# Kernel tuning notes

Hardware: AMD Instinct MI355X
Metric: run time of the kernel (lower is better)

Reference implementation:

```python
import jax, jax.numpy as jnp
import numpy as np

N, H, V = 8192, 1024, 32000
IGNORE_INDEX = -100
LABEL_SMOOTHING = 0.0
LOGIT_SCALE = 1.0


def setup_inputs() -> dict:
    key = jax.random.key(0)
    k1, k2, k3 = jax.random.split(key, 3)
    x = jax.random.normal(k1, (N, H), dtype=jnp.float32)
    weight = jax.random.normal(k2, (V, H), dtype=jnp.float32) * 0.02
    bias = jnp.zeros((V,), dtype=jnp.float32)
    target = jax.random.randint(k3, (N,), 0, V, dtype=jnp.int64)
    return {"x": x, "weight": weight, "bias": bias, "target": target}


def reference(x, weight, bias, target):
    # logits: [N, V]; fused kernel never materializes this fully, but math is identical
    logits = (x @ weight.T + bias) * LOGIT_SCALE
    lse = jax.nn.logsumexp(logits.astype(jnp.float32), axis=-1)  # [N]
    valid = target != IGNORE_INDEX
    safe_t = jnp.where(valid, target, 0)
    tgt_logit = jnp.take_along_axis(logits, safe_t[:, None], axis=-1)[:, 0]
    loss_i = lse - tgt_logit
    if LABEL_SMOOTHING > 0:
        eps = LABEL_SMOOTHING / V
        z = (-eps * logits).sum(-1)
        loss_i = loss_i * (1.0 - LABEL_SMOOTHING) + (z + LABEL_SMOOTHING * lse)
    loss_i = jnp.where(valid, loss_i, 0.0)
    total = jnp.maximum(valid.sum(), 1)
    # reduction == 'mean': each per-token loss divided by total, then summed
    return loss_i.sum() / total
```

## Files before the change

kernel.cpp:

```cpp
#include <hip/hip_runtime.h>
#include <math.h>

typedef int    intx8    __attribute__((ext_vector_type(8)));
typedef float  floatx16 __attribute__((ext_vector_type(16)));

#define N_ROWS 8192
#define H_DIM  1024
#define V_DIM  32000
#define V_PAD  32768
#define IGNORE_INDEX (-100)

#define S_SPLITS 16
#define TILES_PER_SPLIT 16
#define BM 256
#define BN 128
#define BK 128

#define LOG2E 1.4426950408889634f
#define LN2   0.6931471805599453f

__global__ __launch_bounds__(256) void convert_fp8(const float* __restrict__ in,
                                                   unsigned char* __restrict__ out,
                                                   int Rstride, float scale) {
  const int r = blockIdx.x * 256 + threadIdx.x;
  const int u = blockIdx.y;
  const float4* src = (const float4*)(in + (size_t)r * H_DIM + u * 16);
  uint4 res;
#pragma unroll
  for (int j = 0; j < 4; ++j) {
    const float4 v = src[j];
    int p = __builtin_amdgcn_cvt_pk_fp8_f32(v.x * scale, v.y * scale, 0, false);
    p = __builtin_amdgcn_cvt_pk_fp8_f32(v.z * scale, v.w * scale, p, true);
    ((int*)&res)[j] = p;
  }
  *(uint4*)(out + ((size_t)u * Rstride + r) * 16) = res;
}

__global__ __launch_bounds__(256) void pad_bias(const float* __restrict__ bias,
                                                float* __restrict__ biasp) {
  const int i = blockIdx.x * 256 + threadIdx.x;
  biasp[i] = (i < V_DIM) ? bias[i] * LOG2E : -1e30f;
}

__global__ __launch_bounds__(256, 2) void flce_main(const unsigned char* __restrict__ xs,
                                                    const unsigned char* __restrict__ wsb,
                                                    const float* __restrict__ biasp,
                                                    float* __restrict__ partials) {
  __shared__ __align__(16) unsigned char smA[8 * 256 * 16];
  __shared__ __align__(16) unsigned char smB[8 * 128 * 16];

  const int tid  = threadIdx.x;
  const int lane = tid & 63;
  const int w    = tid >> 6;
  const int l31  = lane & 31;
  const int half = lane >> 5;
  const int wr   = w * 64;
  const int row0 = blockIdx.x * BM;
  const int sidx = blockIdx.y;

  float l_state[32];
#pragma unroll
  for (int i = 0; i < 32; ++i) l_state[i] = 0.f;

#pragma unroll 1
  for (int ct = 0; ct < TILES_PER_SPLIT; ++ct) {
    const int n0 = (sidx * TILES_PER_SPLIT + ct) * BN;
    floatx16 acc[2][4];
#pragma unroll
    for (int mb = 0; mb < 2; ++mb)
#pragma unroll
      for (int nb = 0; nb < 4; ++nb)
#pragma unroll
        for (int i = 0; i < 16; ++i) acc[mb][nb][i] = 0.f;

#pragma unroll 1
    for (int k0i = 0; k0i < H_DIM / BK; ++k0i) {
      const int ub = k0i * 8;
      __syncthreads();
#pragma unroll
      for (int j = 0; j < 8; ++j) {
        const int c = j * 4 + w;
        const int u = c >> 2;
        const int rb = c & 3;
        __builtin_amdgcn_global_load_lds(
            (const __attribute__((address_space(1))) void*)(xs + ((size_t)(ub + u) * N_ROWS + row0 + rb * 64 + lane) * 16),
            (__attribute__((address_space(3))) void*)(smA + ((u * 256 + rb * 64 + lane) * 16)),
            16, 0, 0);
      }
#pragma unroll
      for (int j = 0; j < 4; ++j) {
        const int c = j * 4 + w;
        const int u = c >> 1;
        const int rb = c & 1;
        __builtin_amdgcn_global_load_lds(
            (const __attribute__((address_space(1))) void*)(wsb + ((size_t)(ub + u) * V_PAD + n0 + rb * 64 + lane) * 16),
            (__attribute__((address_space(3))) void*)(smB + ((u * 128 + rb * 64 + lane) * 16)),
            16, 0, 0);
      }
      __syncthreads();

#pragma unroll
      for (int s2 = 0; s2 < 2; ++s2) {
        const int ua = s2 * 4 + half * 2;
        union { intx8 v; uint4 q[2]; } a[2], b[4];
#pragma unroll
        for (int mb = 0; mb < 2; ++mb) {
          a[mb].q[0] = *(const uint4*)(smA + ((ua * 256 + wr + mb * 32 + l31) * 16));
          a[mb].q[1] = *(const uint4*)(smA + (((ua + 1) * 256 + wr + mb * 32 + l31) * 16));
        }
#pragma unroll
        for (int nb = 0; nb < 4; ++nb) {
          b[nb].q[0] = *(const uint4*)(smB + ((ua * 128 + nb * 32 + l31) * 16));
          b[nb].q[1] = *(const uint4*)(smB + (((ua + 1) * 128 + nb * 32 + l31) * 16));
        }
#pragma unroll
        for (int mb = 0; mb < 2; ++mb)
#pragma unroll
          for (int nb = 0; nb < 4; ++nb)
            acc[mb][nb] = __builtin_amdgcn_mfma_scale_f32_32x32x64_f8f6f4(
                a[mb].v, b[nb].v, acc[mb][nb],
                0, 0,
                0, 0x7F7F7F7F,
                0, 0x7F7F7F7F);
      }
    }

    float bnb[4];
#pragma unroll
    for (int nb = 0; nb < 4; ++nb) bnb[nb] = biasp[n0 + nb * 32 + l31];
#pragma unroll
    for (int mb = 0; mb < 2; ++mb)
#pragma unroll
      for (int r = 0; r < 16; ++r) {
        float s = exp2f(acc[mb][0][r] + bnb[0]) + exp2f(acc[mb][1][r] + bnb[1])
                + exp2f(acc[mb][2][r] + bnb[2]) + exp2f(acc[mb][3][r] + bnb[3]);
        l_state[mb * 16 + r] += s;
      }
  }

#pragma unroll
  for (int s = 0; s < 32; ++s) {
    float v = l_state[s];
#pragma unroll
    for (int off = 1; off < 32; off <<= 1) v += __shfl_xor(v, off, 64);
    l_state[s] = v;
  }

  if (l31 == 0) {
#pragma unroll
    for (int s = 0; s < 32; ++s) {
      const int mb = s >> 4, r = s & 15;
      const int row = wr + mb * 32 + 4 * half + (r & 3) + 8 * (r >> 2);
      partials[(size_t)(row0 + row) * S_SPLITS + sidx] = l_state[s];
    }
  }
}

__global__ __launch_bounds__(256) void tgt_kernel(const float* __restrict__ x,
                                                  const float* __restrict__ wgt,
                                                  const float* __restrict__ bias,
                                                  const int* __restrict__ target,
                                                  float* __restrict__ tgt_logit) {
  const int r = blockIdx.x * 4 + (threadIdx.x >> 6);
  const int lane = threadIdx.x & 63;
  const int t = target[r];
  const int tt = (t == IGNORE_INDEX) ? 0 : t;
  const float4* xr = (const float4*)(x + (size_t)r * H_DIM);
  const float4* wr = (const float4*)(wgt + (size_t)tt * H_DIM);
  float acc = 0.f;
#pragma unroll
  for (int i = 0; i < 4; ++i) {
    const float4 a = xr[lane + i * 64];
    const float4 b = wr[lane + i * 64];
    acc += a.x * b.x + a.y * b.y + a.z * b.z + a.w * b.w;
  }
#pragma unroll
  for (int off = 32; off >= 1; off >>= 1) acc += __shfl_xor(acc, off, 64);
  if (lane == 0) tgt_logit[r] = acc + bias[tt];
}

__global__ __launch_bounds__(256) void loss_rows(const float* __restrict__ partials,
                                                 const float* __restrict__ tgt_logit,
                                                 const int* __restrict__ target,
                                                 float* __restrict__ bsums) {
  const int r = blockIdx.x * 256 + threadIdx.x;
  float l = 0.f;
#pragma unroll
  for (int s = 0; s < S_SPLITS; ++s) l += partials[(size_t)r * S_SPLITS + s];
  const float lse = LN2 * __log2f(l);
  const bool valid = (target[r] != IGNORE_INDEX);
  float loss = valid ? (lse - tgt_logit[r]) : 0.f;
  float cnt  = valid ? 1.f : 0.f;
  const int lane = threadIdx.x & 63;
  const int w = threadIdx.x >> 6;
#pragma unroll
  for (int off = 32; off >= 1; off >>= 1) {
    loss += __shfl_xor(loss, off, 64);
    cnt  += __shfl_xor(cnt, off, 64);
  }
  __shared__ float sl[4], sc[4];
  if (lane == 0) { sl[w] = loss; sc[w] = cnt; }
  __syncthreads();
  if (threadIdx.x == 0) {
    float S = 0.f, C = 0.f;
    for (int i = 0; i < 4; ++i) { S += sl[i]; C += sc[i]; }
    bsums[blockIdx.x] = S;
    bsums[32 + blockIdx.x] = C;
  }
}

__global__ void finalize(const float* __restrict__ bsums, float* __restrict__ out) {
  const int t = threadIdx.x;
  float s = (t < 32) ? bsums[t] : 0.f;
  float c = (t < 32) ? bsums[32 + t] : 0.f;
#pragma unroll
  for (int off = 32; off >= 1; off >>= 1) {
    s += __shfl_xor(s, off, 64);
    c += __shfl_xor(c, off, 64);
  }
  if (t == 0) out[0] = s / fmaxf(c, 1.f);
}

extern "C" void kernel_launch(void* const* d_in, const int* in_sizes, int n_in,
                              void* d_out, int out_size, void* d_ws, size_t ws_size,
                              hipStream_t stream) {
  const float* x    = (const float*)d_in[0];
  const float* wgt  = (const float*)d_in[1];
  const float* bias = (const float*)d_in[2];
  const int*   tgt  = (const int*)d_in[3];
  float* out = (float*)d_out;

  char* ws = (char*)d_ws;
  const size_t XS8 = (size_t)N_ROWS * H_DIM;
  const size_t WS8 = (size_t)V_PAD * H_DIM;
  const size_t BP  = (size_t)V_PAD * 4;
  const size_t PB  = (size_t)N_ROWS * S_SPLITS * 4;
  unsigned char* xs8 = (unsigned char*)ws;
  unsigned char* ws8 = (unsigned char*)(ws + XS8);
  float* biasp    = (float*)(ws + XS8 + WS8);
  float* partials = (float*)(ws + XS8 + WS8 + BP);
  float* tgt_lg   = (float*)(ws + XS8 + WS8 + BP + PB);
  float* bsums    = (float*)(ws + XS8 + WS8 + BP + PB + (size_t)N_ROWS * 4);

  convert_fp8<<<dim3(N_ROWS / 256, H_DIM / 16), 256, 0, stream>>>(x, xs8, N_ROWS, LOG2E);
  convert_fp8<<<dim3(V_DIM / 256, H_DIM / 16), 256, 0, stream>>>(wgt, ws8, V_PAD, 1.0f);
  pad_bias<<<V_PAD / 256, 256, 0, stream>>>(bias, biasp);
  tgt_kernel<<<N_ROWS / 4, 256, 0, stream>>>(x, wgt, bias, tgt, tgt_lg);
  flce_main<<<dim3(N_ROWS / BM, S_SPLITS), 256, 0, stream>>>(xs8, ws8, biasp, partials);
  loss_rows<<<N_ROWS / 256, 256, 0, stream>>>(partials, tgt_lg, tgt, bsums);
  finalize<<<1, 64, 0, stream>>>(bsums, out);
}
```

Baseline: 504.2 us.

## Double-buffer LDS tiles with prefetch two steps ahead across column tiles

Replaces the synchronous load-then-compute K loop with a two-buffer software pipeline using BK=64 steps. Global-to-LDS loads for step+2 are issued right after the current fragments are read into registers, and the pipeline runs continuously across column tiles so loads overlap the MFMAs. It also stages the bias slice into LDS once at kernel start, uses manual vmcnt/lgkmcnt waits with raw barriers, and raises wave priority around the MFMA block. Costs are more barriers per K, a larger LDS footprint that may affect occupancy, and fragile hand-counted wait values.

```diff
diff --git a/kernel.cpp b/kernel.cpp
--- a/kernel.cpp
+++ b/kernel.cpp
@@ -14,7 +14,9 @@
 #define TILES_PER_SPLIT 16
 #define BM 256
 #define BN 128
-#define BK 128
+#define BK 64
+#define KSTEPS 16
+#define TOTAL_STEPS (TILES_PER_SPLIT * KSTEPS)
 
 #define LOG2E 1.4426950408889634f
 #define LN2   0.6931471805599453f
@@ -42,12 +44,86 @@
   biasp[i] = (i < V_DIM) ? bias[i] * LOG2E : -1e30f;
 }
 
+
+#define STAGE(ST, CUR) do {                                                              \
+    const int _ss = (ST);                                                                \
+    const int _ks = _ss & 15;                                                            \
+    const int _ct = _ss >> 4;                                                            \
+    const int _ub = _ks * 4;                                                             \
+    const int _n0 = (sidx * TILES_PER_SPLIT + _ct) * BN;                                 \
+    _Pragma("unroll")                                                                    \
+    for (int _j = 0; _j < 4; ++_j) {                                                     \
+      const int _c = _j * 4 + w, _u = _c >> 2, _rb = _c & 3;                             \
+      __builtin_amdgcn_global_load_lds(                                                  \
+          (const __attribute__((address_space(1))) void*)(xs +                           \
+              ((size_t)(_ub + _u) * N_ROWS + row0 + _rb * 64 + lane) * 16),              \
+          (__attribute__((address_space(3))) void*)(smA + (CUR) * (4 * 256 * 16) +       \
+              (_u * 256 + _rb * 64 + lane) * 16),                                        \
+          16, 0, 0);                                                                     \
+    }                                                                                    \
+    _Pragma("unroll")                                                                    \
+    for (int _j = 0; _j < 2; ++_j) {                                                     \
+      const int _c = _j * 4 + w, _u = _c >> 1, _rb = _c & 1;                             \
+      __builtin_amdgcn_global_load_lds(                                                  \
+          (const __attribute__((address_space(1))) void*)(wsb +                          \
+              ((size_t)(_ub + _u) * V_PAD + _n0 + _rb * 64 + lane) * 16),                \
+          (__attribute__((address_space(3))) void*)(smB + (CUR) * (4 * 128 * 16) +       \
+              (_u * 128 + _rb * 64 + lane) * 16),                                        \
+          16, 0, 0);                                                                     \
+    }                                                                                    \
+  } while (0)
+
+#define DO_STEP(ST, CUR) do {                                                            \
+    const int _st = (ST);                                                                \
+                     \
+    if (_st < TOTAL_STEPS - 1) asm volatile("s_waitcnt vmcnt(6)" ::: "memory");          \
+    else                       asm volatile("s_waitcnt vmcnt(0)" ::: "memory");          \
+    __builtin_amdgcn_sched_barrier(0);                                                   \
+    __builtin_amdgcn_s_barrier();                     \
+    union { intx8 v; uint4 q[2]; } a[2], b[4];                                           \
+    {                                                                                    \
+      const int ua = half * 2;                                                           \
+      _Pragma("unroll")                                                                  \
+      for (int mb = 0; mb < 2; ++mb) {                                                   \
+        a[mb].q[0] = *(const uint4*)(smA + (CUR) * (4 * 256 * 16) +                      \
+                                     ((ua * 256 + wr + mb * 32 + l31) * 16));            \
+        a[mb].q[1] = *(const uint4*)(smA + (CUR) * (4 * 256 * 16) +                      \
+                                     (((ua + 1) * 256 + wr + mb * 32 + l31) * 16));      \
+      }                                                                                  \
+      _Pragma("unroll")                                                                  \
+      for (int nb = 0; nb < 4; ++nb) {                                                   \
+        b[nb].q[0] = *(const uint4*)(smB + (CUR) * (4 * 128 * 16) +                      \
+                                     ((ua * 128 + nb * 32 + l31) * 16));                 \
+        b[nb].q[1] = *(const uint4*)(smB + (CUR) * (4 * 128 * 16) +                      \
+                                     (((ua + 1) * 128 + nb * 32 + l31) * 16));           \
+      }                                                                                  \
+    }                                                                                    \
+    asm volatile("s_waitcnt lgkmcnt(0)" ::: "memory");        \
+    __builtin_amdgcn_sched_barrier(0);                                                   \
+    __builtin_amdgcn_s_barrier();                   \
+    __builtin_amdgcn_sched_barrier(0);                                                   \
+    if (_st + 2 < TOTAL_STEPS) STAGE(_st + 2, CUR);           \
+    __builtin_amdgcn_sched_barrier(0);                                                   \
+    __builtin_amdgcn_s_setprio(1);                                                       \
+    _Pragma("unroll")                                                                    \
+    for (int mb = 0; mb < 2; ++mb)                                                       \
+      _Pragma("unroll")                                                                  \
+      for (int nb = 0; nb < 4; ++nb)                                                     \
+        acc[mb][nb] = __builtin_amdgcn_mfma_scale_f32_32x32x64_f8f6f4(                   \
+            a[mb].v, b[nb].v, acc[mb][nb],                                               \
+            0, 0,                                                  \
+            0, 0x7F7F7F7F,                                            \
+            0, 0x7F7F7F7F);                                           \
+    __builtin_amdgcn_s_setprio(0);                                                       \
+  } while (0)
+
 __global__ __launch_bounds__(256, 2) void flce_main(const unsigned char* __restrict__ xs,
                                                     const unsigned char* __restrict__ wsb,
                                                     const float* __restrict__ biasp,
                                                     float* __restrict__ partials) {
-  __shared__ __align__(16) unsigned char smA[8 * 256 * 16];
-  __shared__ __align__(16) unsigned char smB[8 * 128 * 16];
+  __shared__ __align__(16) unsigned char smA[2 * 4 * 256 * 16];
+  __shared__ __align__(16) unsigned char smB[2 * 4 * 128 * 16];
+  __shared__ __align__(16) float sbias[TILES_PER_SPLIT * BN];
 
   const int tid  = threadIdx.x;
   const int lane = tid & 63;
@@ -62,9 +138,20 @@
 #pragma unroll
   for (int i = 0; i < 32; ++i) l_state[i] = 0.f;
 
+#pragma unroll
+  for (int j = 0; j < 2; ++j) {
+    const int c = j * 4 + w;
+    __builtin_amdgcn_global_load_lds(
+        (const __attribute__((address_space(1))) void*)(biasp +
+            (size_t)sidx * (TILES_PER_SPLIT * BN) + c * 256 + lane * 4),
+        (__attribute__((address_space(3))) void*)(sbias + c * 256 + lane * 4),
+        16, 0, 0);
+  }
+  STAGE(0, 0);
+  STAGE(1, 1);
+
 #pragma unroll 1
   for (int ct = 0; ct < TILES_PER_SPLIT; ++ct) {
-    const int n0 = (sidx * TILES_PER_SPLIT + ct) * BN;
     floatx16 acc[2][4];
 #pragma unroll
     for (int mb = 0; mb < 2; ++mb)
@@ -74,60 +161,15 @@
         for (int i = 0; i < 16; ++i) acc[mb][nb][i] = 0.f;
 
 #pragma unroll 1
-    for (int k0i = 0; k0i < H_DIM / BK; ++k0i) {
-      const int ub = k0i * 8;
-      __syncthreads();
-#pragma unroll
-      for (int j = 0; j < 8; ++j) {
-        const int c = j * 4 + w;
-        const int u = c >> 2;
-        const int rb = c & 3;
-        __builtin_amdgcn_global_load_lds(
-            (const __attribute__((address_space(1))) void*)(xs + ((size_t)(ub + u) * N_ROWS + row0 + rb * 64 + lane) * 16),
-            (__attribute__((address_space(3))) void*)(smA + ((u * 256 + rb * 64 + lane) * 16)),
-            16, 0, 0);
-      }
-#pragma unroll
-      for (int j = 0; j < 4; ++j) {
-        const int c = j * 4 + w;
-        const int u = c >> 1;
-        const int rb = c & 1;
-        __builtin_amdgcn_global_load_lds(
-            (const __attribute__((address_space(1))) void*)(wsb + ((size_t)(ub + u) * V_PAD + n0 + rb * 64 + lane) * 16),
-            (__attribute__((address_space(3))) void*)(smB + ((u * 128 + rb * 64 + lane) * 16)),
-            16, 0, 0);
-      }
-      __syncthreads();
-
-#pragma unroll
-      for (int s2 = 0; s2 < 2; ++s2) {
-        const int ua = s2 * 4 + half * 2;
-        union { intx8 v; uint4 q[2]; } a[2], b[4];
-#pragma unroll
-        for (int mb = 0; mb < 2; ++mb) {
-          a[mb].q[0] = *(const uint4*)(smA + ((ua * 256 + wr + mb * 32 + l31) * 16));
-          a[mb].q[1] = *(const uint4*)(smA + (((ua + 1) * 256 + wr + mb * 32 + l31) * 16));
-        }
-#pragma unroll
-        for (int nb = 0; nb < 4; ++nb) {
-          b[nb].q[0] = *(const uint4*)(smB + ((ua * 128 + nb * 32 + l31) * 16));
-          b[nb].q[1] = *(const uint4*)(smB + (((ua + 1) * 128 + nb * 32 + l31) * 16));
-        }
-#pragma unroll
-        for (int mb = 0; mb < 2; ++mb)
-#pragma unroll
-          for (int nb = 0; nb < 4; ++nb)
-            acc[mb][nb] = __builtin_amdgcn_mfma_scale_f32_32x32x64_f8f6f4(
-                a[mb].v, b[nb].v, acc[mb][nb],
-                0, 0,
-                0, 0x7F7F7F7F,
-                0, 0x7F7F7F7F);
-      }
+    for (int ks2 = 0; ks2 < 8; ++ks2) {
+      const int st0 = ct * 16 + ks2 * 2;
+      DO_STEP(st0, 0);
+      DO_STEP(st0 + 1, 1);
     }
 
     float bnb[4];
 #pragma unroll
-    for (int nb = 0; nb < 4; ++nb) bnb[nb] = biasp[n0 + nb * 32 + l31];
+    for (int nb = 0; nb < 4; ++nb) bnb[nb] = sbias[ct * BN + nb * 32 + l31];
 #pragma unroll
     for (int mb = 0; mb < 2; ++mb)
 #pragma unroll
```

Measured after the change: 548.1 us. +8.7%, slower.

## Triple-buffer LDS loads with one barrier per K-step and prefetch across tiles

Applied to the files above, without the earlier changes.

Replaces the two-barrier, single-buffer K loop with a three-stage LDS ring that uses BK=64 and a single barrier per step. Global-to-LDS loads are issued two steps ahead, including across column-tile boundaries, and synchronisation relies on explicit vmcnt waits. Bias values are preloaded into LDS once per block, and MFMA issue is given raised wave priority. The aim is to hide global load latency behind MFMA work and drop the barrier stalls. In exchange, each step does less compute per barrier and the vmcnt accounting is fragile.

```diff
diff --git a/kernel.cpp b/kernel.cpp
--- a/kernel.cpp
+++ b/kernel.cpp
@@ -14,7 +14,12 @@
 #define TILES_PER_SPLIT 16
 #define BM 256
 #define BN 128
-#define BK 128
+#define BK 64
+#define KSTEPS 16
+#define TOTAL_STEPS (TILES_PER_SPLIT * KSTEPS)
+
+#define ABUF_SZ (4 * 256 * 16)
+#define BBUF_SZ (4 * 128 * 16)
 
 #define LOG2E 1.4426950408889634f
 #define LN2   0.6931471805599453f
@@ -42,12 +47,42 @@
   biasp[i] = (i < V_DIM) ? bias[i] * LOG2E : -1e30f;
 }
 
+
+#define STAGE(ST, BUF) do {                                                              \
+    const int _ss = (ST);                                                                \
+    const int _ks = _ss & 15;                                                            \
+    const int _ct = _ss >> 4;                                                            \
+    const int _ub = _ks * 4;                                                             \
+    const int _n0 = (sidx * TILES_PER_SPLIT + _ct) * BN;                                 \
+    unsigned char* _dA = smA + (BUF) * ABUF_SZ;                                          \
+    unsigned char* _dB = smB + (BUF) * BBUF_SZ;                                          \
+    _Pragma("unroll")                                                                    \
+    for (int _j = 0; _j < 4; ++_j) {                                                     \
+      const int _c = _j * 4 + w, _u = _c >> 2, _rb = _c & 3;                             \
+      __builtin_amdgcn_global_load_lds(                                                  \
+          (const __attribute__((address_space(1))) void*)(xs +                           \
+              ((size_t)(_ub + _u) * N_ROWS + row0 + _rb * 64 + lane) * 16),              \
+          (__attribute__((address_space(3))) void*)(_dA + (_u * 256 + _rb * 64 + lane) * 16), \
+          16, 0, 0);                                                                     \
+    }                                                                                    \
+    _Pragma("unroll")                                                                    \
+    for (int _j = 0; _j < 2; ++_j) {                                                     \
+      const int _c = _j * 4 + w, _u = _c >> 1, _rb = _c & 1;                             \
+      __builtin_amdgcn_global_load_lds(                                                  \
+          (const __attribute__((address_space(1))) void*)(wsb +                          \
+              ((size_t)(_ub + _u) * V_PAD + _n0 + _rb * 64 + lane) * 16),                \
+          (__attribute__((address_space(3))) void*)(_dB + (_u * 128 + _rb * 64 + lane) * 16), \
+          16, 0, 0);                                                                     \
+    }                                                                                    \
+  } while (0)
+
 __global__ __launch_bounds__(256, 2) void flce_main(const unsigned char* __restrict__ xs,
                                                     const unsigned char* __restrict__ wsb,
                                                     const float* __restrict__ biasp,
                                                     float* __restrict__ partials) {
-  __shared__ __align__(16) unsigned char smA[8 * 256 * 16];
-  __shared__ __align__(16) unsigned char smB[8 * 128 * 16];
+  __shared__ __align__(16) unsigned char smA[3 * ABUF_SZ];
+  __shared__ __align__(16) unsigned char smB[3 * BBUF_SZ];
+  __shared__ __align__(16) float sbias[TILES_PER_SPLIT * BN];
 
   const int tid  = threadIdx.x;
   const int lane = tid & 63;
@@ -62,9 +97,22 @@
 #pragma unroll
   for (int i = 0; i < 32; ++i) l_state[i] = 0.f;
 
+#pragma unroll
+  for (int j = 0; j < 2; ++j) {
+    const int c = j * 4 + w;
+    __builtin_amdgcn_global_load_lds(
+        (const __attribute__((address_space(1))) void*)(biasp +
+            (size_t)sidx * (TILES_PER_SPLIT * BN) + c * 256 + lane * 4),
+        (__attribute__((address_space(3))) void*)(sbias + c * 256 + lane * 4),
+        16, 0, 0);
+  }
+  STAGE(0, 0);
+  STAGE(1, 1);
+
+  int b0 = 0, b1 = 1, b2 = 2;
+
 #pragma unroll 1
   for (int ct = 0; ct < TILES_PER_SPLIT; ++ct) {
-    const int n0 = (sidx * TILES_PER_SPLIT + ct) * BN;
     floatx16 acc[2][4];
 #pragma unroll
     for (int mb = 0; mb < 2; ++mb)
@@ -74,60 +122,50 @@
         for (int i = 0; i < 16; ++i) acc[mb][nb][i] = 0.f;
 
 #pragma unroll 1
-    for (int k0i = 0; k0i < H_DIM / BK; ++k0i) {
-      const int ub = k0i * 8;
-      __syncthreads();
-#pragma unroll
-      for (int j = 0; j < 8; ++j) {
-        const int c = j * 4 + w;
-        const int u = c >> 2;
-        const int rb = c & 3;
-        __builtin_amdgcn_global_load_lds(
-            (const __attribute__((address_space(1))) void*)(xs + ((size_t)(ub + u) * N_ROWS + row0 + rb * 64 + lane) * 16),
-            (__attribute__((address_space(3))) void*)(smA + ((u * 256 + rb * 64 + lane) * 16)),
-            16, 0, 0);
+    for (int ks = 0; ks < KSTEPS; ++ks) {
+      const int st = ct * KSTEPS + ks;
+
+      if (st == TOTAL_STEPS - 1) asm volatile("s_waitcnt vmcnt(0)" ::: "memory");
+      else                       asm volatile("s_waitcnt vmcnt(6)" ::: "memory");
+      __builtin_amdgcn_sched_barrier(0);
+      __builtin_amdgcn_s_barrier();
+      __builtin_amdgcn_sched_barrier(0);
+
+      if (st + 2 < TOTAL_STEPS) STAGE(st + 2, b2);
+
+      union { intx8 v; uint4 q[2]; } a[2], b[4];
+      const unsigned char* pA = smA + b0 * ABUF_SZ;
+      const unsigned char* pB = smB + b0 * BBUF_SZ;
+      const int ua = half * 2;
+#pragma unroll
+      for (int mb = 0; mb < 2; ++mb) {
+        a[mb].q[0] = *(const uint4*)(pA + ((ua * 256 + wr + mb * 32 + l31) * 16));
+        a[mb].q[1] = *(const uint4*)(pA + (((ua + 1) * 256 + wr + mb * 32 + l31) * 16));
       }
 #pragma unroll
-      for (int j = 0; j < 4; ++j) {
-        const int c = j * 4 + w;
-        const int u = c >> 1;
-        const int rb = c & 1;
-        __builtin_amdgcn_global_load_lds(
-            (const __attribute__((address_space(1))) void*)(wsb + ((size_t)(ub + u) * V_PAD + n0 + rb * 64 + lane) * 16),
-            (__attribute__((address_space(3))) void*)(smB + ((u * 128 + rb * 64 + lane) * 16)),
-            16, 0, 0);
+      for (int nb = 0; nb < 4; ++nb) {
+        b[nb].q[0] = *(const uint4*)(pB + ((ua * 128 + nb * 32 + l31) * 16));
+        b[nb].q[1] = *(const uint4*)(pB + (((ua + 1) * 128 + nb * 32 + l31) * 16));
       }
-      __syncthreads();
-
-#pragma unroll
-      for (int s2 = 0; s2 < 2; ++s2) {
-        const int ua = s2 * 4 + half * 2;
-        union { intx8 v; uint4 q[2]; } a[2], b[4];
-#pragma unroll
-        for (int mb = 0; mb < 2; ++mb) {
-          a[mb].q[0] = *(const uint4*)(smA + ((ua * 256 + wr + mb * 32 + l31) * 16));
-          a[mb].q[1] = *(const uint4*)(smA + (((ua + 1) * 256 + wr + mb * 32 + l31) * 16));
-        }
-#pragma unroll
-        for (int nb = 0; nb < 4; ++nb) {
-          b[nb].q[0] = *(const uint4*)(smB + ((ua * 128 + nb * 32 + l31) * 16));
-          b[nb].q[1] = *(const uint4*)(smB + (((ua + 1) * 128 + nb * 32 + l31) * 16));
-        }
-#pragma unroll
-        for (int mb = 0; mb < 2; ++mb)
-#pragma unroll
-          for (int nb = 0; nb < 4; ++nb)
-            acc[mb][nb] = __builtin_amdgcn_mfma_scale_f32_32x32x64_f8f6f4(
-                a[mb].v, b[nb].v, acc[mb][nb],
-                0, 0,
-                0, 0x7F7F7F7F,
-                0, 0x7F7F7F7F);
-      }
+
+      __builtin_amdgcn_s_setprio(1);
+#pragma unroll
+      for (int mb = 0; mb < 2; ++mb)
+#pragma unroll
+        for (int nb = 0; nb < 4; ++nb)
+          acc[mb][nb] = __builtin_amdgcn_mfma_scale_f32_32x32x64_f8f6f4(
+              a[mb].v, b[nb].v, acc[mb][nb],
+              0, 0,
+              0, 0x7F7F7F7F,
+              0, 0x7F7F7F7F);
+      __builtin_amdgcn_s_setprio(0);
+
+      const int bt = b0; b0 = b1; b1 = b2; b2 = bt;
     }
 
     float bnb[4];
 #pragma unroll
-    for (int nb = 0; nb < 4; ++nb) bnb[nb] = biasp[n0 + nb * 32 + l31];
+    for (int nb = 0; nb < 4; ++nb) bnb[nb] = sbias[ct * BN + nb * 32 + l31];
 #pragma unroll
     for (int mb = 0; mb < 2; ++mb)
 #pragma unroll
```

Result: slower. 544.3 us (+8.0%).

## Double-buffer weight tiles in LDS and load activation fragments directly from global

Applied to the files above, without the earlier changes.

Weight (B) tiles now stream into a two-slot LDS buffer, with the next k-step's tile prefetched before the current one is computed. That leaves one barrier per step where there used to be two. Activation (A) fragments skip LDS and are read per-lane straight from global memory, which also halves LDS use and can let more blocks fit. Wave priority is raised around the MFMA bursts. The risk is that the direct global A loads expose latency and re-read A from L2 on every column tile.

```diff
diff --git a/kernel.cpp b/kernel.cpp
--- a/kernel.cpp
+++ b/kernel.cpp
@@ -14,7 +14,9 @@
 #define TILES_PER_SPLIT 16
 #define BM 256
 #define BN 128
-#define BK 128
+#define KSTEPS 8
+#define TOTAL_STEPS (TILES_PER_SPLIT * KSTEPS)
+#define BBUF (8 * 128 * 16)
 
 #define LOG2E 1.4426950408889634f
 #define LN2   0.6931471805599453f
@@ -42,29 +44,52 @@
   biasp[i] = (i < V_DIM) ? bias[i] * LOG2E : -1e30f;
 }
 
+
+typedef union { intx8 v; uint4 q[2]; } frag;
+
+#define BDMA(T) do {                                                                     \
+    const int _t = (T);                                                                  \
+    const int _ub = (_t & 7) * 8;                                                        \
+    const int _n0 = (sidx * TILES_PER_SPLIT + (_t >> 3)) * BN;                           \
+    unsigned char* _d = smB + ((_t & 1) ? BBUF : 0);                                     \
+    _Pragma("unroll")                                                                    \
+    for (int _j = 0; _j < 4; ++_j) {                                                     \
+      const int _c = _j * 4 + w, _u = _c >> 1, _rb = _c & 1;                             \
+      __builtin_amdgcn_global_load_lds(                                                  \
+          (const __attribute__((address_space(1))) void*)(wsb +                          \
+              ((size_t)(_ub + _u) * V_PAD + _n0 + _rb * 64 + lane) * 16),                \
+          (__attribute__((address_space(3))) void*)(_d + ((_u * 128 + _rb * 64 + lane) * 16)), \
+          16, 0, 0);                                                                     \
+    }                                                                                    \
+  } while (0)
+
 __global__ __launch_bounds__(256, 2) void flce_main(const unsigned char* __restrict__ xs,
                                                     const unsigned char* __restrict__ wsb,
                                                     const float* __restrict__ biasp,
                                                     float* __restrict__ partials) {
-  __shared__ __align__(16) unsigned char smA[8 * 256 * 16];
-  __shared__ __align__(16) unsigned char smB[8 * 128 * 16];
+  __shared__ __align__(16) unsigned char smB[2 * BBUF];
 
   const int tid  = threadIdx.x;
   const int lane = tid & 63;
   const int w    = tid >> 6;
   const int l31  = lane & 31;
   const int half = lane >> 5;
+  const int half2 = half * 2;
   const int wr   = w * 64;
   const int row0 = blockIdx.x * BM;
   const int sidx = blockIdx.y;
 
+  const size_t arow0 = (size_t)(row0 + wr + l31);
+  const size_t arow1 = arow0 + 32;
+
   float l_state[32];
 #pragma unroll
   for (int i = 0; i < 32; ++i) l_state[i] = 0.f;
+
+  BDMA(0);
 
 #pragma unroll 1
   for (int ct = 0; ct < TILES_PER_SPLIT; ++ct) {
-    const int n0 = (sidx * TILES_PER_SPLIT + ct) * BN;
     floatx16 acc[2][4];
 #pragma unroll
     for (int mb = 0; mb < 2; ++mb)
@@ -74,57 +99,66 @@
         for (int i = 0; i < 16; ++i) acc[mb][nb][i] = 0.f;
 
 #pragma unroll 1
-    for (int k0i = 0; k0i < H_DIM / BK; ++k0i) {
+    for (int k0i = 0; k0i < KSTEPS; ++k0i) {
+      const int st = ct * KSTEPS + k0i;
       const int ub = k0i * 8;
+
       __syncthreads();
-#pragma unroll
-      for (int j = 0; j < 8; ++j) {
-        const int c = j * 4 + w;
-        const int u = c >> 2;
-        const int rb = c & 3;
-        __builtin_amdgcn_global_load_lds(
-            (const __attribute__((address_space(1))) void*)(xs + ((size_t)(ub + u) * N_ROWS + row0 + rb * 64 + lane) * 16),
-            (__attribute__((address_space(3))) void*)(smA + ((u * 256 + rb * 64 + lane) * 16)),
-            16, 0, 0);
-      }
-#pragma unroll
-      for (int j = 0; j < 4; ++j) {
-        const int c = j * 4 + w;
-        const int u = c >> 1;
-        const int rb = c & 1;
-        __builtin_amdgcn_global_load_lds(
-            (const __attribute__((address_space(1))) void*)(wsb + ((size_t)(ub + u) * V_PAD + n0 + rb * 64 + lane) * 16),
-            (__attribute__((address_space(3))) void*)(smB + ((u * 128 + rb * 64 + lane) * 16)),
-            16, 0, 0);
-      }
-      __syncthreads();
-
-#pragma unroll
-      for (int s2 = 0; s2 < 2; ++s2) {
-        const int ua = s2 * 4 + half * 2;
-        union { intx8 v; uint4 q[2]; } a[2], b[4];
-#pragma unroll
-        for (int mb = 0; mb < 2; ++mb) {
-          a[mb].q[0] = *(const uint4*)(smA + ((ua * 256 + wr + mb * 32 + l31) * 16));
-          a[mb].q[1] = *(const uint4*)(smA + (((ua + 1) * 256 + wr + mb * 32 + l31) * 16));
+      if (st + 1 < TOTAL_STEPS) BDMA(st + 1);
+
+      frag aK0[2], aK1[2];
+      {
+        const size_t u0 = (size_t)(ub + half2);
+        const size_t u1 = (size_t)(ub + 4 + half2);
+        aK0[0].q[0] = *(const uint4*)(xs + ((u0 * N_ROWS + arow0) * 16));
+        aK0[0].q[1] = *(const uint4*)(xs + (((u0 + 1) * N_ROWS + arow0) * 16));
+        aK0[1].q[0] = *(const uint4*)(xs + ((u0 * N_ROWS + arow1) * 16));
+        aK0[1].q[1] = *(const uint4*)(xs + (((u0 + 1) * N_ROWS + arow1) * 16));
+        aK1[0].q[0] = *(const uint4*)(xs + ((u1 * N_ROWS + arow0) * 16));
+        aK1[0].q[1] = *(const uint4*)(xs + (((u1 + 1) * N_ROWS + arow0) * 16));
+        aK1[1].q[0] = *(const uint4*)(xs + ((u1 * N_ROWS + arow1) * 16));
+        aK1[1].q[1] = *(const uint4*)(xs + (((u1 + 1) * N_ROWS + arow1) * 16));
+      }
+
+      const unsigned char* pB = smB + ((st & 1) ? BBUF : 0);
+
+      {
+        frag b[4];
+#pragma unroll
+        for (int nb = 0; nb < 4; ++nb) {
+          b[nb].q[0] = *(const uint4*)(pB + (((half2    ) * 128 + nb * 32 + l31) * 16));
+          b[nb].q[1] = *(const uint4*)(pB + (((half2 + 1) * 128 + nb * 32 + l31) * 16));
         }
-#pragma unroll
-        for (int nb = 0; nb < 4; ++nb) {
-          b[nb].q[0] = *(const uint4*)(smB + ((ua * 128 + nb * 32 + l31) * 16));
-          b[nb].q[1] = *(const uint4*)(smB + (((ua + 1) * 128 + nb * 32 + l31) * 16));
-        }
+        __builtin_amdgcn_s_setprio(1);
 #pragma unroll
         for (int mb = 0; mb < 2; ++mb)
 #pragma unroll
           for (int nb = 0; nb < 4; ++nb)
             acc[mb][nb] = __builtin_amdgcn_mfma_scale_f32_32x32x64_f8f6f4(
-                a[mb].v, b[nb].v, acc[mb][nb],
-                0, 0,
-                0, 0x7F7F7F7F,
-                0, 0x7F7F7F7F);
+                aK0[mb].v, b[nb].v, acc[mb][nb],
+                0, 0, 0, 0x7F7F7F7F, 0, 0x7F7F7F7F);
+        __builtin_amdgcn_s_setprio(0);
+      }
+      {
+        frag b[4];
+#pragma unroll
+        for (int nb = 0; nb < 4; ++nb) {
+          b[nb].q[0] = *(const uint4*)(pB + (((4 + half2) * 128 + nb * 32 + l31) * 16));
+          b[nb].q[1] = *(const uint4*)(pB + (((5 + half2) * 128 + nb * 32 + l31) * 16));
+        }
+        __builtin_amdgcn_s_setprio(1);
+#pragma unroll
+        for (int mb = 0; mb < 2; ++mb)
+#pragma unroll
+          for (int nb = 0; nb < 4; ++nb)
+            acc[mb][nb] = __builtin_amdgcn_mfma_scale_f32_32x32x64_f8f6f4(
+                aK1[mb].v, b[nb].v, acc[mb][nb],
+                0, 0, 0, 0x7F7F7F7F, 0, 0x7F7F7F7F);
+        __builtin_amdgcn_s_setprio(0);
       }
     }
 
+    const int n0 = (sidx * TILES_PER_SPLIT + ct) * BN;
     float bnb[4];
 #pragma unroll
     for (int nb = 0; nb < 4; ++nb) bnb[nb] = biasp[n0 + nb * 32 + l31];
```

Measured after the change: 495.7 us. Within noise of the previous version (-1.7%).
